# Performance work log

Measured on AMD Instinct MI355X. Metric: run time of the kernel, lower is better.

The kernel has to match this reference:

```python
import jax, jax.numpy as jnp
import numpy as np

N_NODES = 50000
N_EDGES = 800000
IN_DIM = 100
HID = 128
OUT = 128
EPS = 1e-5


def setup_inputs() -> dict:
    key = jax.random.key(0)
    ks = jax.random.split(key, 12)
    x = jax.random.normal(ks[0], (N_NODES, IN_DIM), dtype=jnp.float32)
    edge_index = jax.random.randint(ks[1], (2, N_EDGES), 0, N_NODES, dtype=jnp.int32)
    def lin(k, i, o):
        return jax.random.normal(k, (i, o), dtype=jnp.float32) * (1.0 / np.sqrt(i))
    return {
        "x": x,
        "edge_index": edge_index,
        "W_l0": lin(ks[2], IN_DIM, HID),  # neighbor transform, layer 0
        "b_l0": jnp.zeros((HID,), jnp.float32),
        "W_r0": lin(ks[3], IN_DIM, HID),  # root transform, layer 0
        "gamma0": jnp.ones((HID,), jnp.float32),
        "beta0": jnp.zeros((HID,), jnp.float32),
        "W_l1": lin(ks[4], HID, OUT),
        "b_l1": jnp.zeros((OUT,), jnp.float32),
        "W_r1": lin(ks[5], HID, OUT),
        "gamma1": jnp.ones((OUT,), jnp.float32),
        "beta1": jnp.zeros((OUT,), jnp.float32),
    }


def _sage_conv(x, edge_index, W_l, b_l, W_r):
    # PyG SAGEConv (mean aggr): out = lin_l(mean_{j->i} x_j) + lin_r(x_i)
    src, dst = edge_index[0], edge_index[1]
    n = x.shape[0]
    msg_sum = jax.ops.segment_sum(x[src], dst, num_segments=n)        # [N, d_in]
    cnt = jax.ops.segment_sum(jnp.ones((src.shape[0],), x.dtype), dst, num_segments=n)
    agg = msg_sum / jnp.maximum(cnt, 1.0)[:, None]
    return agg @ W_l + b_l + x @ W_r


def _batch_norm(x, gamma, beta):
    # BatchNorm1d with batch statistics (training-mode math, biased var)
    mean = x.mean(axis=0)
    var = x.var(axis=0)
    return gamma * (x - mean) / jnp.sqrt(var + EPS) + beta


def reference(x, edge_index, W_l0, b_l0, W_r0, gamma0, beta0, W_l1, b_l1, W_r1, gamma1, beta1):
    # Layer 0: SAGEConv -> BN -> ReLU (dropout off for determinism)
    h = _sage_conv(x, edge_index, W_l0, b_l0, W_r0)
    h = jax.nn.relu(_batch_norm(h, gamma0, beta0))
    # Layer 1 (last): SAGEConv -> BN
    h = _sage_conv(h, edge_index, W_l1, b_l1, W_r1)
    return _batch_norm(h, gamma1, beta1)
```

## Files before the change

### kernel.cpp

```cpp
#include <hip/hip_runtime.h>
#include <hip/hip_bf16.h>

#define N_NODES 50000
#define N_EDGES 800000
#define BSHIFT  5
#define BUCKS   1563
#define NPAD    50016
#define BSTRIDE 1024
#define BCAP    1024
#define IN_DIM  100
#define HID     128
#define BN_EPS  1e-5f
#define NSLICE  32

typedef unsigned int uint;
typedef unsigned short u16;
typedef __attribute__((ext_vector_type(8))) unsigned short us8;
typedef __attribute__((ext_vector_type(8))) short s8;
typedef __attribute__((ext_vector_type(16))) float f16v;

__device__ __forceinline__ u16 f2bf(float f) {
    uint u = __builtin_bit_cast(uint, f);
    uint r = (u + 0x7FFFu + ((u >> 16) & 1u)) >> 16;
    return (u16)r;
}
__device__ __forceinline__ uint pack2(float a, float b) {
    return (uint)f2bf(a) | ((uint)f2bf(b) << 16);
}
__device__ __forceinline__ float bflo(uint p) { return __builtin_bit_cast(float, p << 16); }
__device__ __forceinline__ float bfhi(uint p) { return __builtin_bit_cast(float, p & 0xFFFF0000u); }

__global__ __launch_bounds__(1024) void bucket_scatter_blk(
    const int* __restrict__ src, const int* __restrict__ dst,
    int* __restrict__ bcursor, uint* __restrict__ ebuf) {
    __shared__ int h[BUCKS];
    __shared__ int gb[BUCKS];
    int t = threadIdx.x;
    for (int i = t; i < BUCKS; i += 1024) h[i] = 0;
    __syncthreads();
    int base = blockIdx.x * 8192;
    int myb[8]; uint myv[8];
    #pragma unroll
    for (int r = 0; r < 8; ++r) {
        int e = base + r * 1024 + t;
        int b = -1; uint val = 0;
        if (e < N_EDGES) {
            int d = dst[e];
            b = d >> BSHIFT;
            val = (uint)src[e] | ((uint)(d & 31) << 16);
            atomicAdd(&h[b], 1);
        }
        myb[r] = b; myv[r] = val;
    }
    __syncthreads();
    for (int i = t; i < BUCKS; i += 1024) {
        int c = h[i];
        gb[i] = c ? (i * BSTRIDE + atomicAdd(&bcursor[i], c)) : 0;
        h[i] = 0;
    }
    __syncthreads();
    #pragma unroll
    for (int r = 0; r < 8; ++r) {
        int b = myb[r];
        if (b >= 0) {
            int pos = gb[b] + atomicAdd(&h[b], 1);
            ebuf[pos] = myv[r];
        }
    }
}

__global__ void cast_all(const float* __restrict__ x,
                         const float* __restrict__ W_l0, const float* __restrict__ W_r0,
                         const float* __restrict__ W_l1, const float* __restrict__ W_r1,
                         u16* __restrict__ xb, u16* __restrict__ Wt) {
    int idx = blockIdx.x * 256 + threadIdx.x;
    if (idx < NPAD * 128) {
        int row = idx >> 7, k = idx & 127;
        float v = (row < N_NODES && k < IN_DIM) ? x[row * IN_DIM + k] : 0.f;
        xb[idx] = f2bf(v);
        return;
    }
    int i2 = idx - NPAD * 128;
    if (i2 >= 4 * 16384) return;
    int w = i2 >> 14, i3 = i2 & 16383;
    const float* s = (w == 0) ? W_l0 : (w == 1) ? W_r0 : (w == 2) ? W_l1 : W_r1;
    int Ks = (w < 2) ? IN_DIM : HID;
    int n = i3 >> 7, k = i3 & 127;
    float v = (k < Ks) ? s[k * 128 + n] : 0.f;
    Wt[i2] = f2bf(v);
}

template <int WRITE_BF16>
__global__ __launch_bounds__(256) void agg_gemm(
    const uint* __restrict__ ebuf, const int* __restrict__ bcursor,
    const u16* __restrict__ X,
    const u16* __restrict__ WtL, const u16* __restrict__ WtR,
    const float* __restrict__ bias,
    float* __restrict__ outf, u16* __restrict__ outb,
    float* __restrict__ gstats) {
    __shared__ u16 Aagg[32][136];
    __shared__ uint eL[BCAP];
    __shared__ u16 srcL[BCAP];
    __shared__ int cnt[32], ro[33], cur[32];
    __shared__ float s1L[128], s2L[128];

    int b = blockIdx.x;
    int t = threadIdx.x;
    int row0 = b * 32;
    int wave = t >> 6, lane = t & 63;
    int quad = lane >> 4, sub = lane & 15;

    int n = bcursor[b];
    if (n > BCAP) n = BCAP;
    if (t < 32) cnt[t] = 0;
    if (t < 128) { s1L[t] = 0.f; s2L[t] = 0.f; }
    __syncthreads();
    for (int i = t; i < n; i += 256) {
        uint p = ebuf[b * BSTRIDE + i];
        eL[i] = p;
        atomicAdd(&cnt[p >> 16], 1);
    }
    __syncthreads();
    if (t < 32) {
        int v = cnt[t];
        int s = v;
        #pragma unroll
        for (int off = 1; off < 32; off <<= 1) {
            int u = __shfl_up(s, off, 64);
            if (t >= off) s += u;
        }
        ro[t] = s - v;
        cur[t] = s - v;
        if (t == 31) ro[32] = s;
    }
    __syncthreads();
    for (int i = t; i < n; i += 256) {
        uint p = eL[i];
        int pos = atomicAdd(&cur[p >> 16], 1);
        srcL[pos] = (u16)(p & 0xFFFFu);
    }
    __syncthreads();

    int nl0 = (wave * 4 + quad) * 2;
    #pragma unroll
    for (int g = 0; g < 2; ++g) {
        int nl = nl0 + g;
        int rb = ro[nl], re = ro[nl + 1];
        float a0 = 0.f, a1 = 0.f, a2 = 0.f, a3 = 0.f;
        float a4 = 0.f, a5 = 0.f, a6 = 0.f, a7 = 0.f;
        int e = rb;
        for (; e + 4 <= re; e += 4) {
            int s0 = srcL[e], s1 = srcL[e + 1], s2 = srcL[e + 2], s3 = srcL[e + 3];
            uint4 v0 = ((const uint4*)(X + (size_t)s0 * 128))[sub];
            uint4 v1 = ((const uint4*)(X + (size_t)s1 * 128))[sub];
            uint4 v2 = ((const uint4*)(X + (size_t)s2 * 128))[sub];
            uint4 v3 = ((const uint4*)(X + (size_t)s3 * 128))[sub];
            a0 += (bflo(v0.x) + bflo(v1.x)) + (bflo(v2.x) + bflo(v3.x));
            a1 += (bfhi(v0.x) + bfhi(v1.x)) + (bfhi(v2.x) + bfhi(v3.x));
            a2 += (bflo(v0.y) + bflo(v1.y)) + (bflo(v2.y) + bflo(v3.y));
            a3 += (bfhi(v0.y) + bfhi(v1.y)) + (bfhi(v2.y) + bfhi(v3.y));
            a4 += (bflo(v0.z) + bflo(v1.z)) + (bflo(v2.z) + bflo(v3.z));
            a5 += (bfhi(v0.z) + bfhi(v1.z)) + (bfhi(v2.z) + bfhi(v3.z));
            a6 += (bflo(v0.w) + bflo(v1.w)) + (bflo(v2.w) + bflo(v3.w));
            a7 += (bfhi(v0.w) + bfhi(v1.w)) + (bfhi(v2.w) + bfhi(v3.w));
        }
        for (; e < re; ++e) {
            uint4 v0 = ((const uint4*)(X + (size_t)srcL[e] * 128))[sub];
            a0 += bflo(v0.x); a1 += bfhi(v0.x);
            a2 += bflo(v0.y); a3 += bfhi(v0.y);
            a4 += bflo(v0.z); a5 += bfhi(v0.z);
            a6 += bflo(v0.w); a7 += bfhi(v0.w);
        }
        float inv = 1.0f / fmaxf((float)(re - rb), 1.0f);
        uint4 o;
        o.x = pack2(a0 * inv, a1 * inv);
        o.y = pack2(a2 * inv, a3 * inv);
        o.z = pack2(a4 * inv, a5 * inv);
        o.w = pack2(a6 * inv, a7 * inv);
        *(uint4*)&Aagg[nl][sub * 8] = o;
    }
    __syncthreads();

    int m31 = lane & 31;
    int kh  = lane >> 5;
    int cn = wave * 32;
    f16v acc = (f16v)0.f;

    {
        s8 a_nxt = *(const s8*)&Aagg[m31][kh * 8];
        s8 b_nxt = *(const s8*)(WtL + (cn + m31) * 128 + kh * 8);
        #pragma unroll
        for (int ks = 0; ks < 8; ++ks) {
            s8 a_cur = a_nxt, b_cur = b_nxt;
            if (ks < 7) {
                a_nxt = *(const s8*)&Aagg[m31][(ks + 1) * 16 + kh * 8];
                b_nxt = *(const s8*)(WtL + (cn + m31) * 128 + (ks + 1) * 16 + kh * 8);
            }
            acc = __builtin_amdgcn_mfma_f32_32x32x16_bf16(a_cur, b_cur, acc, 0, 0, 0);
        }
    }
    {
        const u16* xrow = X + (size_t)(row0 + m31) * 128;
        s8 a_nxt = *(const s8*)(xrow + kh * 8);
        s8 b_nxt = *(const s8*)(WtR + (cn + m31) * 128 + kh * 8);
        #pragma unroll
        for (int ks = 0; ks < 8; ++ks) {
            s8 a_cur = a_nxt, b_cur = b_nxt;
            if (ks < 7) {
                a_nxt = *(const s8*)(xrow + (ks + 1) * 16 + kh * 8);
                b_nxt = *(const s8*)(WtR + (cn + m31) * 128 + (ks + 1) * 16 + kh * 8);
            }
            acc = __builtin_amdgcn_mfma_f32_32x32x16_bf16(a_cur, b_cur, acc, 0, 0, 0);
        }
    }

    {
        int col = cn + m31;
        float bv = bias[col];
        float s1 = 0.f, s2 = 0.f;
        #pragma unroll
        for (int reg = 0; reg < 16; ++reg) {
            int rowin = (reg & 3) + 8 * (reg >> 2) + 4 * kh;
            int row = row0 + rowin;
            if (row < N_NODES) {
                float v = acc[reg] + bv;
                if (WRITE_BF16)
                    outb[(size_t)row * 128 + col] = f2bf(v);
                else
                    outf[(size_t)row * 128 + col] = v;
                s1 += v;
                s2 = fmaf(v, v, s2);
            }
        }
        s1 += __shfl_xor(s1, 32, 64);
        s2 += __shfl_xor(s2, 32, 64);
        if (lane < 32) {
            atomicAdd(&s1L[col], s1);
            atomicAdd(&s2L[col], s2);
        }
    }
    __syncthreads();
    int slice = b & (NSLICE - 1);
    if (t < 128) {
        atomicAdd(&gstats[slice * 256 + t], s1L[t]);
        atomicAdd(&gstats[slice * 256 + 128 + t], s2L[t]);
    }
}

__global__ void bn_relu_inplace(u16* __restrict__ hb,
                                const float* __restrict__ gstats,
                                const float* __restrict__ gamma,
                                const float* __restrict__ beta,
                                float inv_n, int totalv) {
    __shared__ float ss[256];
    int t = threadIdx.x;
    if (t < 128) {
        float m = 0.f, q = 0.f;
        #pragma unroll
        for (int s = 0; s < NSLICE; ++s) {
            m += gstats[s * 256 + t];
            q += gstats[s * 256 + 128 + t];
        }
        float mean = m * inv_n;
        float var = q * inv_n - mean * mean;
        float inv = 1.0f / sqrtf(var + BN_EPS);
        float sc = gamma[t] * inv;
        ss[t] = sc;
        ss[128 + t] = beta[t] - mean * sc;
    }
    __syncthreads();
    for (int i = blockIdx.x * 256 + t; i < totalv; i += gridDim.x * 256) {
        int cg = (i & 15) * 8;
        uint4 p = ((const uint4*)hb)[i];
        float4 scA = *(const float4*)&ss[cg];
        float4 scB = *(const float4*)&ss[cg + 4];
        float4 shA = *(const float4*)&ss[128 + cg];
        float4 shB = *(const float4*)&ss[128 + cg + 4];
        float r0 = fmaxf(fmaf(bflo(p.x), scA.x, shA.x), 0.f);
        float r1 = fmaxf(fmaf(bfhi(p.x), scA.y, shA.y), 0.f);
        float r2 = fmaxf(fmaf(bflo(p.y), scA.z, shA.z), 0.f);
        float r3 = fmaxf(fmaf(bfhi(p.y), scA.w, shA.w), 0.f);
        float r4 = fmaxf(fmaf(bflo(p.z), scB.x, shB.x), 0.f);
        float r5 = fmaxf(fmaf(bfhi(p.z), scB.y, shB.y), 0.f);
        float r6 = fmaxf(fmaf(bflo(p.w), scB.z, shB.z), 0.f);
        float r7 = fmaxf(fmaf(bfhi(p.w), scB.w, shB.w), 0.f);
        uint4 o;
        o.x = pack2(r0, r1);
        o.y = pack2(r2, r3);
        o.z = pack2(r4, r5);
        o.w = pack2(r6, r7);
        ((uint4*)hb)[i] = o;
    }
}

__global__ void bn_apply_kernel(float* __restrict__ h,
                                const float* __restrict__ gstats,
                                const float* __restrict__ gamma,
                                const float* __restrict__ beta,
                                float inv_n, int total4) {
    __shared__ float ss[256];
    int t = threadIdx.x;
    if (t < 128) {
        float m = 0.f, q = 0.f;
        #pragma unroll
        for (int s = 0; s < NSLICE; ++s) {
            m += gstats[s * 256 + t];
            q += gstats[s * 256 + 128 + t];
        }
        float mean = m * inv_n;
        float var = q * inv_n - mean * mean;
        float inv = 1.0f / sqrtf(var + BN_EPS);
        float sc = gamma[t] * inv;
        ss[t] = sc;
        ss[128 + t] = beta[t] - mean * sc;
    }
    __syncthreads();
    for (int i = blockIdx.x * 256 + t; i < total4; i += gridDim.x * 256) {
        int cg = i & 31;
        float4 v = ((float4*)h)[i];
        float4 sc = *(const float4*)&ss[cg * 4];
        float4 sh = *(const float4*)&ss[128 + cg * 4];
        v.x = fmaf(v.x, sc.x, sh.x);
        v.y = fmaf(v.y, sc.y, sh.y);
        v.z = fmaf(v.z, sc.z, sh.z);
        v.w = fmaf(v.w, sc.w, sh.w);
        ((float4*)h)[i] = v;
    }
}

extern "C" void kernel_launch(void* const* d_in, const int* in_sizes, int n_in,
                              void* d_out, int out_size, void* d_ws, size_t ws_size,
                              hipStream_t stream) {
    const float* x      = (const float*)d_in[0];
    const int*   ei     = (const int*)d_in[1];
    const float* W_l0   = (const float*)d_in[2];
    const float* b_l0   = (const float*)d_in[3];
    const float* W_r0   = (const float*)d_in[4];
    const float* gamma0 = (const float*)d_in[5];
    const float* beta0  = (const float*)d_in[6];
    const float* W_l1   = (const float*)d_in[7];
    const float* b_l1   = (const float*)d_in[8];
    const float* W_r1   = (const float*)d_in[9];
    const float* gamma1 = (const float*)d_in[10];
    const float* beta1  = (const float*)d_in[11];

    const int* src = ei;
    const int* dst = ei + N_EDGES;

    char* w = (char*)d_ws;
    auto alloc = [&](size_t bytes) {
        void* p = (void*)w;
        w += (bytes + 255) & ~(size_t)255;
        return p;
    };
    char* zbase    = w;
    float* gstats0 = (float*)alloc(sizeof(float) * NSLICE * 256);
    float* gstats1 = (float*)alloc(sizeof(float) * NSLICE * 256);
    int* bcursor   = (int*)alloc(sizeof(int) * BUCKS);
    size_t zbytes  = (size_t)(w - zbase);

    uint* ebuf     = (uint*)alloc(sizeof(uint) * (size_t)BUCKS * BSTRIDE);
    u16* xb        = (u16*)alloc(sizeof(u16) * (size_t)NPAD * 128);
    u16* hb        = (u16*)alloc(sizeof(u16) * (size_t)NPAD * 128);
    u16* Wt        = (u16*)alloc(sizeof(u16) * 4 * 16384);
    float* outp    = (float*)d_out;

    hipMemsetAsync(zbase, 0, zbytes, stream);

    const float inv_n = 1.0f / (float)N_NODES;
    const int total4 = N_NODES * HID / 4;
    const int totalv = N_NODES * HID / 8;
    const int castN = NPAD * 128 + 4 * 16384;

    bucket_scatter_blk<<<(N_EDGES + 8191) / 8192, 1024, 0, stream>>>(src, dst, bcursor, ebuf);
    cast_all<<<(castN + 255) / 256, 256, 0, stream>>>(x, W_l0, W_r0, W_l1, W_r1, xb, Wt);

    agg_gemm<1><<<BUCKS, 256, 0, stream>>>(ebuf, bcursor, xb, Wt, Wt + 16384, b_l0,
                                           nullptr, hb, gstats0);
    bn_relu_inplace<<<1024, 256, 0, stream>>>(hb, gstats0, gamma0, beta0, inv_n, totalv);

    agg_gemm<0><<<BUCKS, 256, 0, stream>>>(ebuf, bcursor, hb, Wt + 2 * 16384, Wt + 3 * 16384,
                                           b_l1, outp, nullptr, gstats1);
    bn_apply_kernel<<<2048, 256, 0, stream>>>(outp, gstats1, gamma1, beta1, inv_n, total4);
}
```

Baseline: 220.9 us.

## Split fused aggregate+GEMM into sort, feature-sliced aggregation, and GEMM kernels

Moves the per-bucket counting sort into a separate bucket_sort kernel that runs once and is reused by both layers. Aggregation becomes its own kernel launched with 8 feature slices per bucket (64-thread blocks), writing the mean-aggregated rows to a bf16 global buffer. A separate GEMM kernel stages both the aggregated rows and the root rows into LDS before the MFMAs. The aim is more parallelism for the latency-bound gather and no repeated sorting, at the cost of extra launches and a global round trip for the aggregated features.

Result: slower. 318.1 us (+44.0%).

```diff
diff --git a/kernel.cpp b/kernel.cpp
--- a/kernel.cpp
+++ b/kernel.cpp
@@ -69,6 +69,43 @@
     }
 }
 
+__global__ __launch_bounds__(64) void bucket_sort(
+    const uint* __restrict__ ebuf, const int* __restrict__ bcursor,
+    u16* __restrict__ sbuf, int* __restrict__ rob) {
+    __shared__ uint eL[BCAP];
+    __shared__ int cnt[32], ro[33], cur[32];
+    int b = blockIdx.x, t = threadIdx.x;
+    int n = bcursor[b];
+    if (n > BCAP) n = BCAP;
+    if (t < 32) cnt[t] = 0;
+    __syncthreads();
+    for (int i = t; i < n; i += 64) {
+        uint p = ebuf[b * BSTRIDE + i];
+        eL[i] = p;
+        atomicAdd(&cnt[p >> 16], 1);
+    }
+    __syncthreads();
+    if (t < 32) {
+        int v = cnt[t];
+        int s = v;
+        #pragma unroll
+        for (int off = 1; off < 32; off <<= 1) {
+            int u = __shfl_up(s, off, 64);
+            if (t >= off) s += u;
+        }
+        ro[t] = s - v;
+        cur[t] = s - v;
+        if (t == 31) ro[32] = s;
+    }
+    __syncthreads();
+    for (int i = t; i < n; i += 64) {
+        uint p = eL[i];
+        int pos = atomicAdd(&cur[p >> 16], 1);
+        sbuf[b * BSTRIDE + pos] = (u16)(p & 0xFFFFu);
+    }
+    if (t < 33) rob[b * 34 + t] = ro[t];
+}
+
 __global__ void cast_all(const float* __restrict__ x,
                          const float* __restrict__ W_l0, const float* __restrict__ W_r0,
                          const float* __restrict__ W_l1, const float* __restrict__ W_r1,
@@ -90,94 +127,77 @@
     Wt[i2] = f2bf(v);
 }
 
-template <int WRITE_BF16>
-__global__ __launch_bounds__(256) void agg_gemm(
-    const uint* __restrict__ ebuf, const int* __restrict__ bcursor,
-    const u16* __restrict__ X,
-    const u16* __restrict__ WtL, const u16* __restrict__ WtR,
-    const float* __restrict__ bias,
-    float* __restrict__ outf, u16* __restrict__ outb,
-    float* __restrict__ gstats) {
-    __shared__ u16 Aagg[32][136];
-    __shared__ uint eL[BCAP];
-    __shared__ u16 srcL[BCAP];
-    __shared__ int cnt[32], ro[33], cur[32];
-    __shared__ float s1L[128], s2L[128];
-
-    int b = blockIdx.x;
+__global__ __launch_bounds__(64) void agg_sliced(
+    const u16* __restrict__ sbuf, const int* __restrict__ rob,
+    const u16* __restrict__ X, u16* __restrict__ aggb) {
+    int bid = blockIdx.x;
+    int slice = bid & 7;
+    int b = bid >> 3;
     int t = threadIdx.x;
-    int row0 = b * 32;
-    int wave = t >> 6, lane = t & 63;
-    int quad = lane >> 4, sub = lane & 15;
-
-    int n = bcursor[b];
-    if (n > BCAP) n = BCAP;
-    if (t < 32) cnt[t] = 0;
-    if (t < 128) { s1L[t] = 0.f; s2L[t] = 0.f; }
-    __syncthreads();
-    for (int i = t; i < n; i += 256) {
-        uint p = ebuf[b * BSTRIDE + i];
-        eL[i] = p;
-        atomicAdd(&cnt[p >> 16], 1);
-    }
-    __syncthreads();
-    if (t < 32) {
-        int v = cnt[t];
-        int s = v;
-        #pragma unroll
-        for (int off = 1; off < 32; off <<= 1) {
-            int u = __shfl_up(s, off, 64);
-            if (t >= off) s += u;
-        }
-        ro[t] = s - v;
-        cur[t] = s - v;
-        if (t == 31) ro[32] = s;
-    }
-    __syncthreads();
-    for (int i = t; i < n; i += 256) {
-        uint p = eL[i];
-        int pos = atomicAdd(&cur[p >> 16], 1);
-        srcL[pos] = (u16)(p & 0xFFFFu);
-    }
-    __syncthreads();
-
-    int nl0 = (wave * 4 + quad) * 2;
-    #pragma unroll
-    for (int g = 0; g < 2; ++g) {
-        int nl = nl0 + g;
-        int rb = ro[nl], re = ro[nl + 1];
-        float a0 = 0.f, a1 = 0.f, a2 = 0.f, a3 = 0.f;
-        float a4 = 0.f, a5 = 0.f, a6 = 0.f, a7 = 0.f;
-        int e = rb;
-        for (; e + 4 <= re; e += 4) {
-            int s0 = srcL[e], s1 = srcL[e + 1], s2 = srcL[e + 2], s3 = srcL[e + 3];
-            uint4 v0 = ((const uint4*)(X + (size_t)s0 * 128))[sub];
-            uint4 v1 = ((const uint4*)(X + (size_t)s1 * 128))[sub];
-            uint4 v2 = ((const uint4*)(X + (size_t)s2 * 128))[sub];
-            uint4 v3 = ((const uint4*)(X + (size_t)s3 * 128))[sub];
-            a0 += (bflo(v0.x) + bflo(v1.x)) + (bflo(v2.x) + bflo(v3.x));
-            a1 += (bfhi(v0.x) + bfhi(v1.x)) + (bfhi(v2.x) + bfhi(v3.x));
-            a2 += (bflo(v0.y) + bflo(v1.y)) + (bflo(v2.y) + bflo(v3.y));
-            a3 += (bfhi(v0.y) + bfhi(v1.y)) + (bfhi(v2.y) + bfhi(v3.y));
-            a4 += (bflo(v0.z) + bflo(v1.z)) + (bflo(v2.z) + bflo(v3.z));
-            a5 += (bfhi(v0.z) + bfhi(v1.z)) + (bfhi(v2.z) + bfhi(v3.z));
-            a6 += (bflo(v0.w) + bflo(v1.w)) + (bflo(v2.w) + bflo(v3.w));
-            a7 += (bfhi(v0.w) + bfhi(v1.w)) + (bfhi(v2.w) + bfhi(v3.w));
-        }
-        for (; e < re; ++e) {
-            uint4 v0 = ((const uint4*)(X + (size_t)srcL[e] * 128))[sub];
-            a0 += bflo(v0.x); a1 += bfhi(v0.x);
-            a2 += bflo(v0.y); a3 += bfhi(v0.y);
-            a4 += bflo(v0.z); a5 += bfhi(v0.z);
-            a6 += bflo(v0.w); a7 += bfhi(v0.w);
-        }
+    int node = t >> 1, half = t & 1;
+    int rb = rob[b * 34 + node], re = rob[b * 34 + node + 1];
+    const u16* base = X + slice * 16 + half * 8;
+    const u16* sb = sbuf + b * BSTRIDE;
+
+    float a0 = 0.f, a1 = 0.f, a2 = 0.f, a3 = 0.f;
+    float a4 = 0.f, a5 = 0.f, a6 = 0.f, a7 = 0.f;
+    int e = rb;
+    for (; e + 4 <= re; e += 4) {
+        int s0 = sb[e], s1 = sb[e + 1], s2 = sb[e + 2], s3 = sb[e + 3];
+        uint4 v0 = *(const uint4*)(base + (size_t)s0 * 128);
+        uint4 v1 = *(const uint4*)(base + (size_t)s1 * 128);
+        uint4 v2 = *(const uint4*)(base + (size_t)s2 * 128);
+        uint4 v3 = *(const uint4*)(base + (size_t)s3 * 128);
+        a0 += (bflo(v0.x) + bflo(v1.x)) + (bflo(v2.x) + bflo(v3.x));
+        a1 += (bfhi(v0.x) + bfhi(v1.x)) + (bfhi(v2.x) + bfhi(v3.x));
+        a2 += (bflo(v0.y) + bflo(v1.y)) + (bflo(v2.y) + bflo(v3.y));
+        a3 += (bfhi(v0.y) + bfhi(v1.y)) + (bfhi(v2.y) + bfhi(v3.y));
+        a4 += (bflo(v0.z) + bflo(v1.z)) + (bflo(v2.z) + bflo(v3.z));
+        a5 += (bfhi(v0.z) + bfhi(v1.z)) + (bfhi(v2.z) + bfhi(v3.z));
+        a6 += (bflo(v0.w) + bflo(v1.w)) + (bflo(v2.w) + bflo(v3.w));
+        a7 += (bfhi(v0.w) + bfhi(v1.w)) + (bfhi(v2.w) + bfhi(v3.w));
+    }
+    for (; e < re; ++e) {
+        uint4 v0 = *(const uint4*)(base + (size_t)sb[e] * 128);
+        a0 += bflo(v0.x); a1 += bfhi(v0.x);
+        a2 += bflo(v0.y); a3 += bfhi(v0.y);
+        a4 += bflo(v0.z); a5 += bfhi(v0.z);
+        a6 += bflo(v0.w); a7 += bfhi(v0.w);
+    }
+    int gnode = b * 32 + node;
+    if (gnode < N_NODES) {
         float inv = 1.0f / fmaxf((float)(re - rb), 1.0f);
         uint4 o;
         o.x = pack2(a0 * inv, a1 * inv);
         o.y = pack2(a2 * inv, a3 * inv);
         o.z = pack2(a4 * inv, a5 * inv);
         o.w = pack2(a6 * inv, a7 * inv);
-        *(uint4*)&Aagg[nl][sub * 8] = o;
+        *(uint4*)(aggb + (size_t)gnode * 128 + slice * 16 + half * 8) = o;
+    }
+}
+
+template <int WRITE_BF16>
+__global__ __launch_bounds__(256) void gemm_all(
+    const u16* __restrict__ Agg, const u16* __restrict__ X,
+    const u16* __restrict__ WtL, const u16* __restrict__ WtR,
+    const float* __restrict__ bias,
+    float* __restrict__ outf, u16* __restrict__ outb,
+    float* __restrict__ gstats) {
+    __shared__ u16 Aa[32][136];
+    __shared__ u16 Ax[32][136];
+    __shared__ float s1L[128], s2L[128];
+
+    int b = blockIdx.x, t = threadIdx.x;
+    int row0 = b * 32;
+    int wave = t >> 6, lane = t & 63;
+    if (t < 128) { s1L[t] = 0.f; s2L[t] = 0.f; }
+
+    #pragma unroll
+    for (int p = 0; p < 2; ++p) {
+        int idx = p * 256 + t;
+        int r = idx >> 4, c = idx & 15;
+        *(us8*)&Aa[r][c * 8] = *(const us8*)(Agg + (size_t)(row0 + r) * 128 + c * 8);
+        *(us8*)&Ax[r][c * 8] = *(const us8*)(X + (size_t)(row0 + r) * 128 + c * 8);
     }
     __syncthreads();
 
@@ -187,27 +207,26 @@
     f16v acc = (f16v)0.f;
 
     {
-        s8 a_nxt = *(const s8*)&Aagg[m31][kh * 8];
+        s8 a_nxt = *(const s8*)&Aa[m31][kh * 8];
         s8 b_nxt = *(const s8*)(WtL + (cn + m31) * 128 + kh * 8);
         #pragma unroll
         for (int ks = 0; ks < 8; ++ks) {
             s8 a_cur = a_nxt, b_cur = b_nxt;
             if (ks < 7) {
-                a_nxt = *(const s8*)&Aagg[m31][(ks + 1) * 16 + kh * 8];
+                a_nxt = *(const s8*)&Aa[m31][(ks + 1) * 16 + kh * 8];
                 b_nxt = *(const s8*)(WtL + (cn + m31) * 128 + (ks + 1) * 16 + kh * 8);
             }
             acc = __builtin_amdgcn_mfma_f32_32x32x16_bf16(a_cur, b_cur, acc, 0, 0, 0);
         }
     }
     {
-        const u16* xrow = X + (size_t)(row0 + m31) * 128;
-        s8 a_nxt = *(const s8*)(xrow + kh * 8);
+        s8 a_nxt = *(const s8*)&Ax[m31][kh * 8];
         s8 b_nxt = *(const s8*)(WtR + (cn + m31) * 128 + kh * 8);
         #pragma unroll
         for (int ks = 0; ks < 8; ++ks) {
             s8 a_cur = a_nxt, b_cur = b_nxt;
             if (ks < 7) {
-                a_nxt = *(const s8*)(xrow + (ks + 1) * 16 + kh * 8);
+                a_nxt = *(const s8*)&Ax[m31][(ks + 1) * 16 + kh * 8];
                 b_nxt = *(const s8*)(WtR + (cn + m31) * 128 + (ks + 1) * 16 + kh * 8);
             }
             acc = __builtin_amdgcn_mfma_f32_32x32x16_bf16(a_cur, b_cur, acc, 0, 0, 0);
@@ -360,8 +379,11 @@
     size_t zbytes  = (size_t)(w - zbase);
 
     uint* ebuf     = (uint*)alloc(sizeof(uint) * (size_t)BUCKS * BSTRIDE);
+    u16* sbuf      = (u16*)alloc(sizeof(u16) * (size_t)BUCKS * BSTRIDE);
+    int* rob       = (int*)alloc(sizeof(int) * (size_t)BUCKS * 34);
     u16* xb        = (u16*)alloc(sizeof(u16) * (size_t)NPAD * 128);
     u16* hb        = (u16*)alloc(sizeof(u16) * (size_t)NPAD * 128);
+    u16* aggb      = (u16*)alloc(sizeof(u16) * (size_t)NPAD * 128);
     u16* Wt        = (u16*)alloc(sizeof(u16) * 4 * 16384);
     float* outp    = (float*)d_out;
 
@@ -374,12 +396,15 @@
 
     bucket_scatter_blk<<<(N_EDGES + 8191) / 8192, 1024, 0, stream>>>(src, dst, bcursor, ebuf);
     cast_all<<<(castN + 255) / 256, 256, 0, stream>>>(x, W_l0, W_r0, W_l1, W_r1, xb, Wt);
-
-    agg_gemm<1><<<BUCKS, 256, 0, stream>>>(ebuf, bcursor, xb, Wt, Wt + 16384, b_l0,
+    bucket_sort<<<BUCKS, 64, 0, stream>>>(ebuf, bcursor, sbuf, rob);
+
+    agg_sliced<<<BUCKS * 8, 64, 0, stream>>>(sbuf, rob, xb, aggb);
+    gemm_all<1><<<BUCKS, 256, 0, stream>>>(aggb, xb, Wt, Wt + 16384, b_l0,
                                            nullptr, hb, gstats0);
     bn_relu_inplace<<<1024, 256, 0, stream>>>(hb, gstats0, gamma0, beta0, inv_n, totalv);
 
-    agg_gemm<0><<<BUCKS, 256, 0, stream>>>(ebuf, bcursor, hb, Wt + 2 * 16384, Wt + 3 * 16384,
-                                           b_l1, outp, nullptr, gstats1);
+    agg_sliced<<<BUCKS * 8, 64, 0, stream>>>(sbuf, rob, hb, aggb);
+    gemm_all<0><<<BUCKS, 256, 0, stream>>>(aggb, hb, Wt + 2 * 16384, Wt + 3 * 16384, b_l1,
+                                           outp, nullptr, gstats1);
     bn_apply_kernel<<<2048, 256, 0, stream>>>(outp, gstats1, gamma1, beta1, inv_n, total4);
 }
```

## Fuse BN+ReLU into layer-1 gather and merge scatter with cast kernel

Applied to the files above, without the earlier changes.

Removes the standalone BN+ReLU pass over the hidden activations. The second aggregation+GEMM kernel now recomputes BN scale and shift from the layer-0 statistics, and applies normalise+ReLU on the fly to each gathered neighbour row and to the root row feeding the MFMA. Separately, the edge bucket scatter and the bf16 cast of x and the weights are merged into one launch, with different blocks taking each job. This saves a full read and write of the hidden tensor and two launches. In exchange, each of the ~16 neighbour gathers per node now does extra FMA/max work. Rounding also differs slightly, because the hidden state stays un-normalised in bf16 until use.

Result: no change. 217.8 us (-1.4%).

```diff
diff --git a/kernel.cpp b/kernel.cpp
--- a/kernel.cpp
+++ b/kernel.cpp
@@ -13,6 +13,10 @@
 #define BN_EPS  1e-5f
 #define NSLICE  32
 
+#define SC_BLKS 98
+#define CAST_ELEMS (NPAD * 128 + 4 * 16384)
+#define CAST_BLKS ((CAST_ELEMS + 4095) / 4096)
+
 typedef unsigned int uint;
 typedef unsigned short u16;
 typedef __attribute__((ext_vector_type(8))) unsigned short us8;
@@ -29,13 +33,41 @@
 }
 __device__ __forceinline__ float bflo(uint p) { return __builtin_bit_cast(float, p << 16); }
 __device__ __forceinline__ float bfhi(uint p) { return __builtin_bit_cast(float, p & 0xFFFF0000u); }
-
-__global__ __launch_bounds__(1024) void bucket_scatter_blk(
+__device__ __forceinline__ float bfu(u16 v) { return __builtin_bit_cast(float, (uint)v << 16); }
+
+__global__ __launch_bounds__(1024) void scatter_cast(
     const int* __restrict__ src, const int* __restrict__ dst,
-    int* __restrict__ bcursor, uint* __restrict__ ebuf) {
+    int* __restrict__ bcursor, uint* __restrict__ ebuf,
+    const float* __restrict__ x,
+    const float* __restrict__ W_l0, const float* __restrict__ W_r0,
+    const float* __restrict__ W_l1, const float* __restrict__ W_r1,
+    u16* __restrict__ xb, u16* __restrict__ Wt) {
     __shared__ int h[BUCKS];
     __shared__ int gb[BUCKS];
     int t = threadIdx.x;
+
+    if (blockIdx.x >= SC_BLKS) {
+        int base = (blockIdx.x - SC_BLKS) * 4096 + t;
+        #pragma unroll
+        for (int r = 0; r < 4; ++r) {
+            int idx = base + r * 1024;
+            if (idx < NPAD * 128) {
+                int row = idx >> 7, k = idx & 127;
+                float v = (row < N_NODES && k < IN_DIM) ? x[row * IN_DIM + k] : 0.f;
+                xb[idx] = f2bf(v);
+            } else if (idx < CAST_ELEMS) {
+                int i2 = idx - NPAD * 128;
+                int w = i2 >> 14, i3 = i2 & 16383;
+                const float* s = (w == 0) ? W_l0 : (w == 1) ? W_r0 : (w == 2) ? W_l1 : W_r1;
+                int Ks = (w < 2) ? IN_DIM : HID;
+                int n = i3 >> 7, k = i3 & 127;
+                float v = (k < Ks) ? s[k * 128 + n] : 0.f;
+                Wt[i2] = f2bf(v);
+            }
+        }
+        return;
+    }
+
     for (int i = t; i < BUCKS; i += 1024) h[i] = 0;
     __syncthreads();
     int base = blockIdx.x * 8192;
@@ -69,40 +101,23 @@
     }
 }
 
-__global__ void cast_all(const float* __restrict__ x,
-                         const float* __restrict__ W_l0, const float* __restrict__ W_r0,
-                         const float* __restrict__ W_l1, const float* __restrict__ W_r1,
-                         u16* __restrict__ xb, u16* __restrict__ Wt) {
-    int idx = blockIdx.x * 256 + threadIdx.x;
-    if (idx < NPAD * 128) {
-        int row = idx >> 7, k = idx & 127;
-        float v = (row < N_NODES && k < IN_DIM) ? x[row * IN_DIM + k] : 0.f;
-        xb[idx] = f2bf(v);
-        return;
-    }
-    int i2 = idx - NPAD * 128;
-    if (i2 >= 4 * 16384) return;
-    int w = i2 >> 14, i3 = i2 & 16383;
-    const float* s = (w == 0) ? W_l0 : (w == 1) ? W_r0 : (w == 2) ? W_l1 : W_r1;
-    int Ks = (w < 2) ? IN_DIM : HID;
-    int n = i3 >> 7, k = i3 & 127;
-    float v = (k < Ks) ? s[k * 128 + n] : 0.f;
-    Wt[i2] = f2bf(v);
-}
-
-template <int WRITE_BF16>
+template <int APPLY_BN, int WRITE_BF16>
 __global__ __launch_bounds__(256) void agg_gemm(
     const uint* __restrict__ ebuf, const int* __restrict__ bcursor,
     const u16* __restrict__ X,
     const u16* __restrict__ WtL, const u16* __restrict__ WtR,
     const float* __restrict__ bias,
     float* __restrict__ outf, u16* __restrict__ outb,
-    float* __restrict__ gstats) {
+    float* __restrict__ gstats_out,
+    const float* __restrict__ gstats_in,
+    const float* __restrict__ gamma, const float* __restrict__ beta,
+    float inv_n) {
     __shared__ u16 Aagg[32][136];
     __shared__ uint eL[BCAP];
     __shared__ u16 srcL[BCAP];
     __shared__ int cnt[32], ro[33], cur[32];
     __shared__ float s1L[128], s2L[128];
+    __shared__ float ss[256];
 
     int b = blockIdx.x;
     int t = threadIdx.x;
@@ -110,6 +125,21 @@
     int wave = t >> 6, lane = t & 63;
     int quad = lane >> 4, sub = lane & 15;
 
+    if (APPLY_BN && t < 128) {
+        float m = 0.f, q = 0.f;
+        #pragma unroll
+        for (int s = 0; s < NSLICE; ++s) {
+            m += gstats_in[s * 256 + t];
+            q += gstats_in[s * 256 + 128 + t];
+        }
+        float mean = m * inv_n;
+        float var = q * inv_n - mean * mean;
+        float inv = 1.0f / sqrtf(var + BN_EPS);
+        float sc = gamma[t] * inv;
+        ss[t] = sc;
+        ss[128 + t] = beta[t] - mean * sc;
+    }
+
     int n = bcursor[b];
     if (n > BCAP) n = BCAP;
     if (t < 32) cnt[t] = 0;
@@ -141,13 +171,34 @@
     }
     __syncthreads();
 
+    float scr[8], shr[8];
+    if (APPLY_BN) {
+        #pragma unroll
+        for (int j = 0; j < 8; ++j) {
+            scr[j] = ss[sub * 8 + j];
+            shr[j] = ss[128 + sub * 8 + j];
+        }
+    }
     int nl0 = (wave * 4 + quad) * 2;
     #pragma unroll
     for (int g = 0; g < 2; ++g) {
         int nl = nl0 + g;
         int rb = ro[nl], re = ro[nl + 1];
-        float a0 = 0.f, a1 = 0.f, a2 = 0.f, a3 = 0.f;
-        float a4 = 0.f, a5 = 0.f, a6 = 0.f, a7 = 0.f;
+        float a[8];
+        #pragma unroll
+        for (int j = 0; j < 8; ++j) a[j] = 0.f;
+
+        auto acc1 = [&](uint4 v) {
+            float f[8] = { bflo(v.x), bfhi(v.x), bflo(v.y), bfhi(v.y),
+                           bflo(v.z), bfhi(v.z), bflo(v.w), bfhi(v.w) };
+            #pragma unroll
+            for (int j = 0; j < 8; ++j) {
+                float val = f[j];
+                if (APPLY_BN) val = fmaxf(fmaf(val, scr[j], shr[j]), 0.f);
+                a[j] += val;
+            }
+        };
+
         int e = rb;
         for (; e + 4 <= re; e += 4) {
             int s0 = srcL[e], s1 = srcL[e + 1], s2 = srcL[e + 2], s3 = srcL[e + 3];
@@ -155,28 +206,18 @@
             uint4 v1 = ((const uint4*)(X + (size_t)s1 * 128))[sub];
             uint4 v2 = ((const uint4*)(X + (size_t)s2 * 128))[sub];
             uint4 v3 = ((const uint4*)(X + (size_t)s3 * 128))[sub];
-            a0 += (bflo(v0.x) + bflo(v1.x)) + (bflo(v2.x) + bflo(v3.x));
-            a1 += (bfhi(v0.x) + bfhi(v1.x)) + (bfhi(v2.x) + bfhi(v3.x));
-            a2 += (bflo(v0.y) + bflo(v1.y)) + (bflo(v2.y) + bflo(v3.y));
-            a3 += (bfhi(v0.y) + bfhi(v1.y)) + (bfhi(v2.y) + bfhi(v3.y));
-            a4 += (bflo(v0.z) + bflo(v1.z)) + (bflo(v2.z) + bflo(v3.z));
-            a5 += (bfhi(v0.z) + bfhi(v1.z)) + (bfhi(v2.z) + bfhi(v3.z));
-            a6 += (bflo(v0.w) + bflo(v1.w)) + (bflo(v2.w) + bflo(v3.w));
-            a7 += (bfhi(v0.w) + bfhi(v1.w)) + (bfhi(v2.w) + bfhi(v3.w));
+            acc1(v0); acc1(v1); acc1(v2); acc1(v3);
         }
         for (; e < re; ++e) {
             uint4 v0 = ((const uint4*)(X + (size_t)srcL[e] * 128))[sub];
-            a0 += bflo(v0.x); a1 += bfhi(v0.x);
-            a2 += bflo(v0.y); a3 += bfhi(v0.y);
-            a4 += bflo(v0.z); a5 += bfhi(v0.z);
-            a6 += bflo(v0.w); a7 += bfhi(v0.w);
+            acc1(v0);
         }
         float inv = 1.0f / fmaxf((float)(re - rb), 1.0f);
         uint4 o;
-        o.x = pack2(a0 * inv, a1 * inv);
-        o.y = pack2(a2 * inv, a3 * inv);
-        o.z = pack2(a4 * inv, a5 * inv);
-        o.w = pack2(a6 * inv, a7 * inv);
+        o.x = pack2(a[0] * inv, a[1] * inv);
+        o.y = pack2(a[2] * inv, a[3] * inv);
+        o.z = pack2(a[4] * inv, a[5] * inv);
+        o.w = pack2(a[6] * inv, a[7] * inv);
         *(uint4*)&Aagg[nl][sub * 8] = o;
     }
     __syncthreads();
@@ -201,14 +242,27 @@
     }
     {
         const u16* xrow = X + (size_t)(row0 + m31) * 128;
-        s8 a_nxt = *(const s8*)(xrow + kh * 8);
+        us8 a_nxt = *(const us8*)(xrow + kh * 8);
         s8 b_nxt = *(const s8*)(WtR + (cn + m31) * 128 + kh * 8);
         #pragma unroll
         for (int ks = 0; ks < 8; ++ks) {
-            s8 a_cur = a_nxt, b_cur = b_nxt;
+            us8 a_raw = a_nxt;
+            s8 b_cur = b_nxt;
             if (ks < 7) {
-                a_nxt = *(const s8*)(xrow + (ks + 1) * 16 + kh * 8);
+                a_nxt = *(const us8*)(xrow + (ks + 1) * 16 + kh * 8);
                 b_nxt = *(const s8*)(WtR + (cn + m31) * 128 + (ks + 1) * 16 + kh * 8);
+            }
+            s8 a_cur;
+            if (APPLY_BN) {
+                int kb = ks * 16 + kh * 8;
+                #pragma unroll
+                for (int j = 0; j < 8; ++j) {
+                    float f = bfu(a_raw[j]);
+                    f = fmaxf(fmaf(f, ss[kb + j], ss[128 + kb + j]), 0.f);
+                    a_cur[j] = (short)f2bf(f);
+                }
+            } else {
+                a_cur = __builtin_bit_cast(s8, a_raw);
             }
             acc = __builtin_amdgcn_mfma_f32_32x32x16_bf16(a_cur, b_cur, acc, 0, 0, 0);
         }
@@ -242,54 +296,8 @@
     __syncthreads();
     int slice = b & (NSLICE - 1);
     if (t < 128) {
-        atomicAdd(&gstats[slice * 256 + t], s1L[t]);
-        atomicAdd(&gstats[slice * 256 + 128 + t], s2L[t]);
-    }
-}
-
-__global__ void bn_relu_inplace(u16* __restrict__ hb,
-                                const float* __restrict__ gstats,
-                                const float* __restrict__ gamma,
-                                const float* __restrict__ beta,
-                                float inv_n, int totalv) {
-    __shared__ float ss[256];
-    int t = threadIdx.x;
-    if (t < 128) {
-        float m = 0.f, q = 0.f;
-        #pragma unroll
-        for (int s = 0; s < NSLICE; ++s) {
-            m += gstats[s * 256 + t];
-            q += gstats[s * 256 + 128 + t];
-        }
-        float mean = m * inv_n;
-        float var = q * inv_n - mean * mean;
-        float inv = 1.0f / sqrtf(var + BN_EPS);
-        float sc = gamma[t] * inv;
-        ss[t] = sc;
-        ss[128 + t] = beta[t] - mean * sc;
-    }
-    __syncthreads();
-    for (int i = blockIdx.x * 256 + t; i < totalv; i += gridDim.x * 256) {
-        int cg = (i & 15) * 8;
-        uint4 p = ((const uint4*)hb)[i];
-        float4 scA = *(const float4*)&ss[cg];
-        float4 scB = *(const float4*)&ss[cg + 4];
-        float4 shA = *(const float4*)&ss[128 + cg];
-        float4 shB = *(const float4*)&ss[128 + cg + 4];
-        float r0 = fmaxf(fmaf(bflo(p.x), scA.x, shA.x), 0.f);
-        float r1 = fmaxf(fmaf(bfhi(p.x), scA.y, shA.y), 0.f);
-        float r2 = fmaxf(fmaf(bflo(p.y), scA.z, shA.z), 0.f);
-        float r3 = fmaxf(fmaf(bfhi(p.y), scA.w, shA.w), 0.f);
-        float r4 = fmaxf(fmaf(bflo(p.z), scB.x, shB.x), 0.f);
-        float r5 = fmaxf(fmaf(bfhi(p.z), scB.y, shB.y), 0.f);
-        float r6 = fmaxf(fmaf(bflo(p.w), scB.z, shB.z), 0.f);
-        float r7 = fmaxf(fmaf(bfhi(p.w), scB.w, shB.w), 0.f);
-        uint4 o;
-        o.x = pack2(r0, r1);
-        o.y = pack2(r2, r3);
-        o.z = pack2(r4, r5);
-        o.w = pack2(r6, r7);
-        ((uint4*)hb)[i] = o;
+        atomicAdd(&gstats_out[slice * 256 + t], s1L[t]);
+        atomicAdd(&gstats_out[slice * 256 + 128 + t], s2L[t]);
     }
 }
 
@@ -369,17 +377,17 @@
 
     const float inv_n = 1.0f / (float)N_NODES;
     const int total4 = N_NODES * HID / 4;
-    const int totalv = N_NODES * HID / 8;
-    const int castN = NPAD * 128 + 4 * 16384;
-
-    bucket_scatter_blk<<<(N_EDGES + 8191) / 8192, 1024, 0, stream>>>(src, dst, bcursor, ebuf);
-    cast_all<<<(castN + 255) / 256, 256, 0, stream>>>(x, W_l0, W_r0, W_l1, W_r1, xb, Wt);
-
-    agg_gemm<1><<<BUCKS, 256, 0, stream>>>(ebuf, bcursor, xb, Wt, Wt + 16384, b_l0,
-                                           nullptr, hb, gstats0);
-    bn_relu_inplace<<<1024, 256, 0, stream>>>(hb, gstats0, gamma0, beta0, inv_n, totalv);
-
-    agg_gemm<0><<<BUCKS, 256, 0, stream>>>(ebuf, bcursor, hb, Wt + 2 * 16384, Wt + 3 * 16384,
-                                           b_l1, outp, nullptr, gstats1);
+
+    scatter_cast<<<SC_BLKS + CAST_BLKS, 1024, 0, stream>>>(
+        src, dst, bcursor, ebuf, x, W_l0, W_r0, W_l1, W_r1, xb, Wt);
+
+    agg_gemm<0, 1><<<BUCKS, 256, 0, stream>>>(
+        ebuf, bcursor, xb, Wt, Wt + 16384, b_l0,
+        nullptr, hb, gstats0, nullptr, nullptr, nullptr, inv_n);
+
+    agg_gemm<1, 0><<<BUCKS, 256, 0, stream>>>(
+        ebuf, bcursor, hb, Wt + 2 * 16384, Wt + 3 * 16384, b_l1,
+        outp, nullptr, gstats1, gstats0, gamma0, beta0, inv_n);
+
     bn_apply_kernel<<<2048, 256, 0, stream>>>(outp, gstats1, gamma1, beta1, inv_n, total4);
 }
```

## Fuse both SAGE layers and BN into one cooperative persistent kernel

Applied to the files above, without the earlier changes.

Merges the edge bucket scatter and the bf16 cast into a single launch by giving them separate block ranges. The two aggregation+GEMM passes and the BN/ReLU applications now run inside one cooperative kernel of 782 blocks. Each block processes two buckets, and grid-wide syncs replace the kernel boundaries. The aim is to remove launch overhead and the tail gaps between six kernels. The cost is grid.sync latency, lower parallelism per bucket pass (782 blocks instead of 1563), and a fallback path if the cooperative launch fails.

Result: slower. 734.8 us (+232.6%).

```diff
diff --git a/kernel.cpp b/kernel.cpp
--- a/kernel.cpp
+++ b/kernel.cpp
@@ -1,5 +1,8 @@
 #include <hip/hip_runtime.h>
 #include <hip/hip_bf16.h>
+#include <hip/hip_cooperative_groups.h>
+
+namespace cg = cooperative_groups;
 
 #define N_NODES 50000
 #define N_EDGES 800000
@@ -13,6 +16,11 @@
 #define BN_EPS  1e-5f
 #define NSLICE  32
 
+#define COOP_BLKS 782
+#define SC_BLKS 98
+#define CAST_ELEMS (NPAD * 128 + 4 * 16384)
+#define CAST_BLKS ((CAST_ELEMS + 4095) / 4096)
+
 typedef unsigned int uint;
 typedef unsigned short u16;
 typedef __attribute__((ext_vector_type(8))) unsigned short us8;
@@ -30,12 +38,39 @@
 __device__ __forceinline__ float bflo(uint p) { return __builtin_bit_cast(float, p << 16); }
 __device__ __forceinline__ float bfhi(uint p) { return __builtin_bit_cast(float, p & 0xFFFF0000u); }
 
-__global__ __launch_bounds__(1024) void bucket_scatter_blk(
+__global__ __launch_bounds__(1024) void scatter_cast(
     const int* __restrict__ src, const int* __restrict__ dst,
-    int* __restrict__ bcursor, uint* __restrict__ ebuf) {
+    int* __restrict__ bcursor, uint* __restrict__ ebuf,
+    const float* __restrict__ x,
+    const float* __restrict__ W_l0, const float* __restrict__ W_r0,
+    const float* __restrict__ W_l1, const float* __restrict__ W_r1,
+    u16* __restrict__ xb, u16* __restrict__ Wt) {
     __shared__ int h[BUCKS];
     __shared__ int gb[BUCKS];
     int t = threadIdx.x;
+
+    if (blockIdx.x >= SC_BLKS) {
+        int base = (blockIdx.x - SC_BLKS) * 4096 + t;
+        #pragma unroll
+        for (int r = 0; r < 4; ++r) {
+            int idx = base + r * 1024;
+            if (idx < NPAD * 128) {
+                int row = idx >> 7, k = idx & 127;
+                float v = (row < N_NODES && k < IN_DIM) ? x[row * IN_DIM + k] : 0.f;
+                xb[idx] = f2bf(v);
+            } else if (idx < CAST_ELEMS) {
+                int i2 = idx - NPAD * 128;
+                int w = i2 >> 14, i3 = i2 & 16383;
+                const float* s = (w == 0) ? W_l0 : (w == 1) ? W_r0 : (w == 2) ? W_l1 : W_r1;
+                int Ks = (w < 2) ? IN_DIM : HID;
+                int n = i3 >> 7, k = i3 & 127;
+                float v = (k < Ks) ? s[k * 128 + n] : 0.f;
+                Wt[i2] = f2bf(v);
+            }
+        }
+        return;
+    }
+
     for (int i = t; i < BUCKS; i += 1024) h[i] = 0;
     __syncthreads();
     int base = blockIdx.x * 8192;
@@ -69,43 +104,16 @@
     }
 }
 
-__global__ void cast_all(const float* __restrict__ x,
-                         const float* __restrict__ W_l0, const float* __restrict__ W_r0,
-                         const float* __restrict__ W_l1, const float* __restrict__ W_r1,
-                         u16* __restrict__ xb, u16* __restrict__ Wt) {
-    int idx = blockIdx.x * 256 + threadIdx.x;
-    if (idx < NPAD * 128) {
-        int row = idx >> 7, k = idx & 127;
-        float v = (row < N_NODES && k < IN_DIM) ? x[row * IN_DIM + k] : 0.f;
-        xb[idx] = f2bf(v);
-        return;
-    }
-    int i2 = idx - NPAD * 128;
-    if (i2 >= 4 * 16384) return;
-    int w = i2 >> 14, i3 = i2 & 16383;
-    const float* s = (w == 0) ? W_l0 : (w == 1) ? W_r0 : (w == 2) ? W_l1 : W_r1;
-    int Ks = (w < 2) ? IN_DIM : HID;
-    int n = i3 >> 7, k = i3 & 127;
-    float v = (k < Ks) ? s[k * 128 + n] : 0.f;
-    Wt[i2] = f2bf(v);
-}
-
 template <int WRITE_BF16>
-__global__ __launch_bounds__(256) void agg_gemm(
+__device__ __forceinline__ void bucket_pass(
+    int b, int t,
     const uint* __restrict__ ebuf, const int* __restrict__ bcursor,
     const u16* __restrict__ X,
     const u16* __restrict__ WtL, const u16* __restrict__ WtR,
     const float* __restrict__ bias,
     float* __restrict__ outf, u16* __restrict__ outb,
-    float* __restrict__ gstats) {
-    __shared__ u16 Aagg[32][136];
-    __shared__ uint eL[BCAP];
-    __shared__ u16 srcL[BCAP];
-    __shared__ int cnt[32], ro[33], cur[32];
-    __shared__ float s1L[128], s2L[128];
-
-    int b = blockIdx.x;
-    int t = threadIdx.x;
+    u16 (*Aagg)[136], uint* eL, u16* srcL,
+    int* cnt, int* ro, int* cur, float* s1L, float* s2L) {
     int row0 = b * 32;
     int wave = t >> 6, lane = t & 63;
     int quad = lane >> 4, sub = lane & 15;
@@ -113,7 +121,6 @@
     int n = bcursor[b];
     if (n > BCAP) n = BCAP;
     if (t < 32) cnt[t] = 0;
-    if (t < 128) { s1L[t] = 0.f; s2L[t] = 0.f; }
     __syncthreads();
     for (int i = t; i < n; i += 256) {
         uint p = ebuf[b * BSTRIDE + i];
@@ -239,8 +246,143 @@
             atomicAdd(&s2L[col], s2);
         }
     }
-    __syncthreads();
-    int slice = b & (NSLICE - 1);
+}
+
+__global__ __launch_bounds__(256, 4) void fused_layers(
+    const uint* __restrict__ ebuf, const int* __restrict__ bcursor,
+    const u16* __restrict__ xb, u16* __restrict__ hb,
+    const u16* __restrict__ Wt,
+    const float* __restrict__ b_l0, const float* __restrict__ b_l1,
+    const float* __restrict__ gamma0, const float* __restrict__ beta0,
+    const float* __restrict__ gamma1, const float* __restrict__ beta1,
+    float* __restrict__ outp,
+    float* __restrict__ gstats0, float* __restrict__ gstats1,
+    float inv_n) {
+    cg::grid_group grid = cg::this_grid();
+
+    __shared__ u16 Aagg[32][136];
+    __shared__ uint eL[BCAP];
+    __shared__ u16 srcL[BCAP];
+    __shared__ int cnt[32], ro[33], cur[32];
+    __shared__ float s1L[128], s2L[128];
+    __shared__ float ss[256];
+
+    int t = threadIdx.x;
+
+    #pragma unroll 1
+    for (int layer = 0; layer < 2; ++layer) {
+        const u16* X = layer ? hb : xb;
+        const u16* WtL = Wt + (layer * 2) * 16384;
+        const u16* WtR = Wt + (layer * 2 + 1) * 16384;
+        const float* bias = layer ? b_l1 : b_l0;
+        float* gso = layer ? gstats1 : gstats0;
+
+        if (t < 128) { s1L[t] = 0.f; s2L[t] = 0.f; }
+
+        #pragma unroll 1
+        for (int g = 0; g < 2; ++g) {
+            int b = blockIdx.x * 2 + g;
+            if (b < BUCKS) {
+                if (layer == 0)
+                    bucket_pass<1>(b, t, ebuf, bcursor, X, WtL, WtR, bias,
+                                   nullptr, hb, Aagg, eL, srcL, cnt, ro, cur, s1L, s2L);
+                else
+                    bucket_pass<0>(b, t, ebuf, bcursor, X, WtL, WtR, bias,
+                                   outp, nullptr, Aagg, eL, srcL, cnt, ro, cur, s1L, s2L);
+            }
+            __syncthreads();
+        }
+
+        int slice = blockIdx.x & (NSLICE - 1);
+        if (t < 128) {
+            atomicAdd(&gso[slice * 256 + t], s1L[t]);
+            atomicAdd(&gso[slice * 256 + 128 + t], s2L[t]);
+        }
+        __threadfence();
+        grid.sync();
+
+        const float* gs  = layer ? gstats1 : gstats0;
+        const float* gam = layer ? gamma1 : gamma0;
+        const float* bet = layer ? beta1 : beta0;
+        if (t < 128) {
+            float m = 0.f, q = 0.f;
+            #pragma unroll
+            for (int s = 0; s < NSLICE; ++s) {
+                m += gs[s * 256 + t];
+                q += gs[s * 256 + 128 + t];
+            }
+            float mean = m * inv_n;
+            float var = q * inv_n - mean * mean;
+            float inv = 1.0f / sqrtf(var + BN_EPS);
+            float sc = gam[t] * inv;
+            ss[t] = sc;
+            ss[128 + t] = bet[t] - mean * sc;
+        }
+        __syncthreads();
+
+        if (layer == 0) {
+            const int totalv = N_NODES * 16;
+            for (int i = blockIdx.x * 256 + t; i < totalv; i += COOP_BLKS * 256) {
+                int cg2 = (i & 15) * 8;
+                uint4 p = ((const uint4*)hb)[i];
+                float4 scA = *(const float4*)&ss[cg2];
+                float4 scB = *(const float4*)&ss[cg2 + 4];
+                float4 shA = *(const float4*)&ss[128 + cg2];
+                float4 shB = *(const float4*)&ss[128 + cg2 + 4];
+                float r0 = fmaxf(fmaf(bflo(p.x), scA.x, shA.x), 0.f);
+                float r1 = fmaxf(fmaf(bfhi(p.x), scA.y, shA.y), 0.f);
+                float r2 = fmaxf(fmaf(bflo(p.y), scA.z, shA.z), 0.f);
+                float r3 = fmaxf(fmaf(bfhi(p.y), scA.w, shA.w), 0.f);
+                float r4 = fmaxf(fmaf(bflo(p.z), scB.x, shB.x), 0.f);
+                float r5 = fmaxf(fmaf(bfhi(p.z), scB.y, shB.y), 0.f);
+                float r6 = fmaxf(fmaf(bflo(p.w), scB.z, shB.z), 0.f);
+                float r7 = fmaxf(fmaf(bfhi(p.w), scB.w, shB.w), 0.f);
+                uint4 o;
+                o.x = pack2(r0, r1);
+                o.y = pack2(r2, r3);
+                o.z = pack2(r4, r5);
+                o.w = pack2(r6, r7);
+                ((uint4*)hb)[i] = o;
+            }
+            __threadfence();
+            grid.sync();
+            __syncthreads();
+        } else {
+            const int total4 = N_NODES * 32;
+            for (int i = blockIdx.x * 256 + t; i < total4; i += COOP_BLKS * 256) {
+                int cg2 = i & 31;
+                float4 v = ((float4*)outp)[i];
+                float4 sc = *(const float4*)&ss[cg2 * 4];
+                float4 sh = *(const float4*)&ss[128 + cg2 * 4];
+                v.x = fmaf(v.x, sc.x, sh.x);
+                v.y = fmaf(v.y, sc.y, sh.y);
+                v.z = fmaf(v.z, sc.z, sh.z);
+                v.w = fmaf(v.w, sc.w, sh.w);
+                ((float4*)outp)[i] = v;
+            }
+        }
+    }
+}
+
+template <int WRITE_BF16>
+__global__ __launch_bounds__(256) void agg_gemm_nc(
+    const uint* __restrict__ ebuf, const int* __restrict__ bcursor,
+    const u16* __restrict__ X,
+    const u16* __restrict__ WtL, const u16* __restrict__ WtR,
+    const float* __restrict__ bias,
+    float* __restrict__ outf, u16* __restrict__ outb,
+    float* __restrict__ gstats) {
+    __shared__ u16 Aagg[32][136];
+    __shared__ uint eL[BCAP];
+    __shared__ u16 srcL[BCAP];
+    __shared__ int cnt[32], ro[33], cur[32];
+    __shared__ float s1L[128], s2L[128];
+    int t = threadIdx.x;
+    if (t < 128) { s1L[t] = 0.f; s2L[t] = 0.f; }
+    bucket_pass<WRITE_BF16>(blockIdx.x, t, ebuf, bcursor, X, WtL, WtR, bias,
+                            outf, outb, Aagg, eL, srcL, cnt, ro, cur, s1L, s2L);
+    __syncthreads();
+    int slice = blockIdx.x & (NSLICE - 1);
     if (t < 128) {
         atomicAdd(&gstats[slice * 256 + t], s1L[t]);
         atomicAdd(&gstats[slice * 256 + 128 + t], s2L[t]);
@@ -270,12 +412,12 @@
     }
     __syncthreads();
     for (int i = blockIdx.x * 256 + t; i < totalv; i += gridDim.x * 256) {
-        int cg = (i & 15) * 8;
+        int cg2 = (i & 15) * 8;
         uint4 p = ((const uint4*)hb)[i];
-        float4 scA = *(const float4*)&ss[cg];
-        float4 scB = *(const float4*)&ss[cg + 4];
-        float4 shA = *(const float4*)&ss[128 + cg];
-        float4 shB = *(const float4*)&ss[128 + cg + 4];
+        float4 scA = *(const float4*)&ss[cg2];
+        float4 scB = *(const float4*)&ss[cg2 + 4];
+        float4 shA = *(const float4*)&ss[128 + cg2];
+        float4 shB = *(const float4*)&ss[128 + cg2 + 4];
         float r0 = fmaxf(fmaf(bflo(p.x), scA.x, shA.x), 0.f);
         float r1 = fmaxf(fmaf(bfhi(p.x), scA.y, shA.y), 0.f);
         float r2 = fmaxf(fmaf(bflo(p.y), scA.z, shA.z), 0.f);
@@ -316,10 +458,10 @@
     }
     __syncthreads();
     for (int i = blockIdx.x * 256 + t; i < total4; i += gridDim.x * 256) {
-        int cg = i & 31;
+        int cg2 = i & 31;
         float4 v = ((float4*)h)[i];
-        float4 sc = *(const float4*)&ss[cg * 4];
-        float4 sh = *(const float4*)&ss[128 + cg * 4];
+        float4 sc = *(const float4*)&ss[cg2 * 4];
+        float4 sh = *(const float4*)&ss[128 + cg2 * 4];
         v.x = fmaf(v.x, sc.x, sh.x);
         v.y = fmaf(v.y, sc.y, sh.y);
         v.z = fmaf(v.z, sc.z, sh.z);
@@ -367,19 +509,31 @@
 
     hipMemsetAsync(zbase, 0, zbytes, stream);
 
-    const float inv_n = 1.0f / (float)N_NODES;
+    float inv_n = 1.0f / (float)N_NODES;
     const int total4 = N_NODES * HID / 4;
     const int totalv = N_NODES * HID / 8;
-    const int castN = NPAD * 128 + 4 * 16384;
-
-    bucket_scatter_blk<<<(N_EDGES + 8191) / 8192, 1024, 0, stream>>>(src, dst, bcursor, ebuf);
-    cast_all<<<(castN + 255) / 256, 256, 0, stream>>>(x, W_l0, W_r0, W_l1, W_r1, xb, Wt);
-
-    agg_gemm<1><<<BUCKS, 256, 0, stream>>>(ebuf, bcursor, xb, Wt, Wt + 16384, b_l0,
-                                           nullptr, hb, gstats0);
-    bn_relu_inplace<<<1024, 256, 0, stream>>>(hb, gstats0, gamma0, beta0, inv_n, totalv);
-
-    agg_gemm<0><<<BUCKS, 256, 0, stream>>>(ebuf, bcursor, hb, Wt + 2 * 16384, Wt + 3 * 16384,
-                                           b_l1, outp, nullptr, gstats1);
-    bn_apply_kernel<<<2048, 256, 0, stream>>>(outp, gstats1, gamma1, beta1, inv_n, total4);
-}
+
+    scatter_cast<<<SC_BLKS + CAST_BLKS, 1024, 0, stream>>>(
+        src, dst, bcursor, ebuf, x, W_l0, W_r0, W_l1, W_r1, xb, Wt);
+
+    void* args[] = {
+        (void*)&ebuf, (void*)&bcursor, (void*)&xb, (void*)&hb, (void*)&Wt,
+        (void*)&b_l0, (void*)&b_l1,
+        (void*)&gamma0, (void*)&beta0, (void*)&gamma1, (void*)&beta1,
+        (void*)&outp, (void*)&gstats0, (void*)&gstats1, (void*)&inv_n
+    };
+    hipError_t cerr = hipLaunchCooperativeKernel((void*)fused_layers,
+                                                 dim3(COOP_BLKS), dim3(256),
+                                                 args, 0, stream);
+    if (cerr != hipSuccess) {
+        (void)hipGetLastError();
+        agg_gemm_nc<1><<<BUCKS, 256, 0, stream>>>(ebuf, bcursor, xb,
+            Wt, Wt + 16384, b_l0, nullptr, hb, gstats0);
+        bn_relu_inplace<<<1024, 256, 0, stream>>>(hb, gstats0, gamma0, beta0,
+                                                  inv_n, totalv);
+        agg_gemm_nc<0><<<BUCKS, 256, 0, stream>>>(ebuf, bcursor, hb,
+            Wt + 2 * 16384, Wt + 3 * 16384, b_l1, outp, nullptr, gstats1);
+        bn_apply_kernel<<<2048, 256, 0, stream>>>(outp, gstats1, gamma1, beta1,
+                                                  inv_n, total4);
+    }
+}
```
